# Kernel optimization log

Measured on AMD Instinct MI355X. Metric: run time of the kernel, lower is better.

The kernel has to match this reference:

```python
import jax, jax.numpy as jnp
import numpy as np

BN_EPS = 1e-5

def _conv1x1(x, w, b):
    # x: [B,C,H,W], w: [O,C], b: [O] -> [B,O,H,W]
    return jnp.einsum('bchw,oc->bohw', x, w) + b[None, :, None, None]

def setup_inputs() -> dict:
    key = jax.random.key(0)
    ks = jax.random.split(key, 9)
    B, C, H, W = 8, 256, 64, 64
    I = C // 2
    s_in = 1.0 / np.sqrt(C)
    s_out = 1.0 / np.sqrt(I)
    return {
        'x':       jax.random.normal(ks[0], (B, C, H, W), dtype=jnp.float32),
        'g_w':     jax.random.uniform(ks[1], (I, C), jnp.float32, -s_in, s_in),
        'g_b':     jax.random.uniform(ks[2], (I,),  jnp.float32, -s_in, s_in),
        'theta_w': jax.random.uniform(ks[3], (I, C), jnp.float32, -s_in, s_in),
        'theta_b': jax.random.uniform(ks[4], (I,),  jnp.float32, -s_in, s_in),
        'phi_w':   jax.random.uniform(ks[5], (I, C), jnp.float32, -s_in, s_in),
        'phi_b':   jax.random.uniform(ks[6], (I,),  jnp.float32, -s_in, s_in),
        'w_w':     jax.random.uniform(ks[7], (C, I), jnp.float32, -s_out, s_out),
        'w_b':     jax.random.uniform(ks[8], (C,),  jnp.float32, -s_out, s_out),
        'gamma':   jnp.ones((C,), dtype=jnp.float32),   # BN weight init constant 1
        'beta':    jnp.zeros((C,), dtype=jnp.float32),  # BN bias init constant 0
    }

def reference(x, g_w, g_b, theta_w, theta_b, phi_w, phi_b, w_w, w_b, gamma, beta):
    B, C, H, W = x.shape
    I = g_w.shape[0]
    N = H * W
    g_x     = _conv1x1(x, g_w, g_b).reshape(B, I, N)          # [B,I,N]
    theta_x = _conv1x1(x, theta_w, theta_b).reshape(B, I, N)  # [B,I,N]
    phi_x   = _conv1x1(x, phi_w, phi_b).reshape(B, I, N)      # [B,I,N]
    # f = theta^T @ phi : [B,N,N]
    f = jnp.einsum('bin,bim->bnm', theta_x, phi_x)
    a = jax.nn.softmax(f, axis=-1)
    # y = a @ g^T : [B,N,I] -> [B,I,H,W]
    y = jnp.einsum('bnm,bim->bin', a, g_x).reshape(B, I, H, W)
    wy = _conv1x1(y, w_w, w_b)                                # [B,C,H,W]
    # BatchNorm2d (training mode: batch statistics over B,H,W per channel)
    mean = jnp.mean(wy, axis=(0, 2, 3), keepdims=True)
    var = jnp.var(wy, axis=(0, 2, 3), keepdims=True)
    wy_bn = (wy - mean) * jax.lax.rsqrt(var + BN_EPS)
    wy_bn = wy_bn * gamma[None, :, None, None] + beta[None, :, None, None]
    return wy_bn + x
```

## Files before the change

kernel.cpp:

```cpp
#include <hip/hip_runtime.h>

#define B_ 8
#define C_ 256
#define I_ 128
#define N_ 4096
#define BN_ (B_ * N_)
#define LOG2E 1.4426950408889634f

typedef __attribute__((ext_vector_type(8))) short bf16x8;
typedef __attribute__((ext_vector_type(4))) float f32x4;
typedef __attribute__((ext_vector_type(4))) int i32x4;

static __device__ __forceinline__ short f2bf(float f) {
    unsigned u = __float_as_uint(f);
    unsigned r = u + 0x7fffu + ((u >> 16) & 1u);
    return (short)(r >> 16);
}
static __device__ __forceinline__ float bf2f(short s) {
    return __uint_as_float(((unsigned)(unsigned short)s) << 16);
}
static __device__ __forceinline__ unsigned cvt_pk_bf16(float lo, float hi) {
    unsigned r;
    asm("v_cvt_pk_bf16_f32 %0, %1, %2" : "=v"(r) : "v"(lo), "v"(hi));
    return r;
}

__global__ void k_prep(const float* g_w, const float* theta_w, const float* phi_w,
                       const float* g_b, const float* theta_b, const float* phi_b,
                       const float* w_w, short* wcat, short* wwb, float* bcat) {
    int i = blockIdx.x * 256 + threadIdx.x;
    if (i < 384 * 256) {
        int j = i >> 8, c = i & 255;
        float v = (j < 128) ? theta_w[j * 256 + c] * LOG2E
                : (j < 256) ? phi_w[(j - 128) * 256 + c]
                            : g_w[(j - 256) * 256 + c];
        wcat[i] = f2bf(v);
    } else if (i < 384 * 256 + 256 * 128) {
        int k = i - 384 * 256;
        wwb[k] = f2bf(w_w[k]);
    } else if (i < 384 * 256 + 256 * 128 + 384) {
        int j = i - (384 * 256 + 256 * 128);
        bcat[j] = (j < 128) ? theta_b[j] * LOG2E
                : (j < 256) ? phi_b[j - 128] : g_b[j - 256];
    }
}

__global__ __launch_bounds__(256) void k_proj(const float* __restrict__ x,
                                              const short* __restrict__ wcat,
                                              const float* __restrict__ bcat,
                                              short* __restrict__ tp,
                                              short* __restrict__ gmat) {
    int b = blockIdx.y;
    int n0 = blockIdx.x * 64;
    int tid = threadIdx.x;
    int wave = tid >> 6, lane = tid & 63, s = lane & 15, q = lane >> 4;
    __shared__ short xs[64][264];

#pragma unroll
    for (int it = 0; it < 16; ++it) {
        int cr = (tid >> 4) + it * 16;
        int nc = tid & 15;
        const float4 v = *(const float4*)&x[((size_t)b * C_ + cr) * N_ + n0 + nc * 4];
        xs[nc * 4 + 0][cr] = f2bf(v.x);
        xs[nc * 4 + 1][cr] = f2bf(v.y);
        xs[nc * 4 + 2][cr] = f2bf(v.z);
        xs[nc * 4 + 3][cr] = f2bf(v.w);
    }
    __syncthreads();

    f32x4 acc[4][6];
#pragma unroll
    for (int rt = 0; rt < 4; ++rt)
#pragma unroll
        for (int jt = 0; jt < 6; ++jt) acc[rt][jt] = (f32x4){0.f, 0.f, 0.f, 0.f};

#pragma unroll
    for (int kb = 0; kb < 8; ++kb) {
        bf16x8 af[4], bfv[6];
#pragma unroll
        for (int rt = 0; rt < 4; ++rt)
            af[rt] = *(const bf16x8*)&xs[rt * 16 + s][kb * 32 + q * 8];
#pragma unroll
        for (int jt = 0; jt < 6; ++jt)
            bfv[jt] = *(const bf16x8*)&wcat[(wave * 96 + jt * 16 + s) * 256 + kb * 32 + q * 8];
#pragma unroll
        for (int rt = 0; rt < 4; ++rt)
#pragma unroll
            for (int jt = 0; jt < 6; ++jt)
                acc[rt][jt] = __builtin_amdgcn_mfma_f32_16x16x32_bf16(af[rt], bfv[jt], acc[rt][jt], 0, 0, 0);
    }

#pragma unroll
    for (int rt = 0; rt < 4; ++rt)
#pragma unroll
        for (int jt = 0; jt < 6; ++jt) {
            int j = wave * 96 + jt * 16 + s;
            float bias = bcat[j];
#pragma unroll
            for (int r = 0; r < 4; ++r) {
                int n = n0 + rt * 16 + 4 * q + r;
                float v = acc[rt][jt][r] + bias;
                if (j < 256)
                    tp[((size_t)b * N_ + n) * 256 + j] = f2bf(v);
                else
                    gmat[((size_t)b * I_ + (j - 256)) * N_ + n] = f2bf(v);
            }
        }
}

__global__ __launch_bounds__(256, 2) void k_attn(const short* __restrict__ tp,
                                                 const short* __restrict__ gmat,
                                                 float* __restrict__ Op,
                                                 float* __restrict__ lbuf) {
    int id = blockIdx.x;
    int b = id & 7;
    int qt = (id >> 3) & 31;
    int half = id >> 8;
    int n0 = qt * 128;
    int tid = threadIdx.x;
    int wave = tid >> 6, lane = tid & 63, s = lane & 15, q = lane >> 4;

    __shared__ __align__(16) short Kt[128 * 128];
    __shared__ __align__(16) short Vt[128 * 128];

    char* KtB = (char*)Kt;
    char* VtB = (char*)Vt;

    const int swz = (s & 7) << 4;
    int kA[4];
#pragma unroll
    for (int kb = 0; kb < 4; ++kb) kA[kb] = s * 256 + ((kb * 64 + q * 16) ^ swz);
    int vA[2];
#pragma unroll
    for (int kb2 = 0; kb2 < 2; ++kb2)
        vA[kb2] = s * 256 + ((kb2 * 64 + q * 16) ^ swz);
    int krow = tid >> 4, kch = tid & 15;
    int stW = krow * 256 + ((kch * 16) ^ ((krow & 7) << 4));

    bf16x8 qf[2][4];
#pragma unroll
    for (int fr = 0; fr < 2; ++fr) {
        const short* qb = tp + ((size_t)b * N_ + n0 + wave * 32 + fr * 16 + s) * 256;
#pragma unroll
        for (int kb = 0; kb < 4; ++kb) qf[fr][kb] = *(const bf16x8*)(qb + kb * 32 + q * 8);
    }

    f32x4 ot[2][8];
#pragma unroll
    for (int fr = 0; fr < 2; ++fr)
#pragma unroll
        for (int t = 0; t < 8; ++t) ot[fr][t] = (f32x4){0.f, 0.f, 0.f, 0.f};
    float lsum[2] = {0.f, 0.f};

    const int mStart = half * 2048, mEnd = mStart + 2048;

    bf16x8 pk[8], pv[8];
#pragma unroll
    for (int it = 0; it < 8; ++it) {
        pk[it] = *(const bf16x8*)&tp[((size_t)b * N_ + mStart + krow + it * 16) * 256 + 128 + kch * 8];
        pv[it] = *(const bf16x8*)&gmat[((size_t)b * I_ + krow + it * 16) * N_ + mStart + kch * 8];
    }

    for (int m0 = mStart; m0 < mEnd; m0 += 128) {
        __syncthreads();
#pragma unroll
        for (int it = 0; it < 8; ++it) {
            *(bf16x8*)(KtB + stW + it * 4096) = pk[it];
            *(bf16x8*)(VtB + stW + it * 4096) = pv[it];
        }
        __syncthreads();
        if (m0 + 128 < mEnd) {
#pragma unroll
            for (int it = 0; it < 8; ++it) {
                pk[it] = *(const bf16x8*)&tp[((size_t)b * N_ + m0 + 128 + krow + it * 16) * 256 + 128 + kch * 8];
                pv[it] = *(const bf16x8*)&gmat[((size_t)b * I_ + krow + it * 16) * N_ + m0 + 128 + kch * 8];
            }
        }

#pragma unroll
        for (int h = 0; h < 2; ++h) {
            const int hK = h * 16384;
            const int hV = h * 128;

            f32x4 sa[2][4];
#pragma unroll
            for (int fr = 0; fr < 2; ++fr)
#pragma unroll
                for (int tc = 0; tc < 4; ++tc) sa[fr][tc] = (f32x4){0.f, 0.f, 0.f, 0.f};
            __builtin_amdgcn_s_setprio(1);
#pragma unroll
            for (int tc = 0; tc < 4; ++tc) {
                bf16x8 bfv[4];
#pragma unroll
                for (int kb = 0; kb < 4; ++kb)
                    bfv[kb] = *(const bf16x8*)(KtB + hK + kA[kb] + tc * 4096);
#pragma unroll
                for (int fr = 0; fr < 2; ++fr)
#pragma unroll
                    for (int kb = 0; kb < 4; ++kb)
                        sa[fr][tc] = __builtin_amdgcn_mfma_f32_16x16x32_bf16(bfv[kb], qf[fr][kb], sa[fr][tc], 0, 0, 0);
            }
            __builtin_amdgcn_s_setprio(0);

            unsigned W[2][4][2];
#pragma unroll
            for (int fr = 0; fr < 2; ++fr) {
#pragma unroll
                for (int tc = 0; tc < 4; ++tc)
#pragma unroll
                    for (int r = 0; r < 4; ++r) sa[fr][tc][r] = exp2f(sa[fr][tc][r]);
                float t0 = (sa[fr][0][0] + sa[fr][0][1]) + (sa[fr][0][2] + sa[fr][0][3]);
                float t1 = (sa[fr][1][0] + sa[fr][1][1]) + (sa[fr][1][2] + sa[fr][1][3]);
                float t2 = (sa[fr][2][0] + sa[fr][2][1]) + (sa[fr][2][2] + sa[fr][2][3]);
                float t3 = (sa[fr][3][0] + sa[fr][3][1]) + (sa[fr][3][2] + sa[fr][3][3]);
                lsum[fr] += (t0 + t1) + (t2 + t3);
#pragma unroll
                for (int tc = 0; tc < 4; ++tc) {
                    W[fr][tc][0] = cvt_pk_bf16(sa[fr][tc][0], sa[fr][tc][1]);
                    W[fr][tc][1] = cvt_pk_bf16(sa[fr][tc][2], sa[fr][tc][3]);
                }
            }

#pragma unroll
            for (int kb2 = 0; kb2 < 2; ++kb2) {
                bf16x8 pa[2];
#pragma unroll
                for (int fr = 0; fr < 2; ++fr) {
                    unsigned rA = W[fr][2 * kb2 + 0][0];
                    unsigned rB = W[fr][2 * kb2 + 0][1];
                    unsigned rC = W[fr][2 * kb2 + 1][0];
                    unsigned rD = W[fr][2 * kb2 + 1][1];
                    asm("v_permlane32_swap_b32 %0, %1" : "+v"(rA), "+v"(rC));
                    asm("v_permlane32_swap_b32 %0, %1" : "+v"(rB), "+v"(rD));
                    asm("v_permlane16_swap_b32 %0, %1" : "+v"(rA), "+v"(rC));
                    asm("v_permlane16_swap_b32 %0, %1" : "+v"(rB), "+v"(rD));
                    i32x4 wv = (i32x4){(int)rA, (int)rB, (int)rC, (int)rD};
                    pa[fr] = __builtin_bit_cast(bf16x8, wv);
                }
                __builtin_amdgcn_s_setprio(1);
#pragma unroll
                for (int t = 0; t < 8; ++t) {
                    bf16x8 vb = *(const bf16x8*)(VtB + hV + vA[kb2] + t * 4096);
                    ot[0][t] = __builtin_amdgcn_mfma_f32_16x16x32_bf16(pa[0], vb, ot[0][t], 0, 0, 0);
                    ot[1][t] = __builtin_amdgcn_mfma_f32_16x16x32_bf16(pa[1], vb, ot[1][t], 0, 0, 0);
                }
                __builtin_amdgcn_s_setprio(0);
            }
        }
    }

#pragma unroll
    for (int fr = 0; fr < 2; ++fr) {
        lsum[fr] += __shfl_xor(lsum[fr], 16);
        lsum[fr] += __shfl_xor(lsum[fr], 32);
    }
    if (q == 0) {
#pragma unroll
        for (int fr = 0; fr < 2; ++fr) {
            size_t row = (size_t)half * BN_ + (size_t)b * N_ + n0 + wave * 32 + fr * 16 + s;
            lbuf[row] = lsum[fr];
        }
    }

#pragma unroll
    for (int fr = 0; fr < 2; ++fr) {
        size_t rbase = (size_t)half * BN_ + (size_t)b * N_ + n0 + wave * 32 + fr * 16 + 4 * q;
#pragma unroll
        for (int t = 0; t < 8; ++t)
#pragma unroll
            for (int r = 0; r < 4; ++r)
                Op[(rbase + r) * I_ + t * 16 + s] = ot[fr][t][r];
    }
}

__global__ __launch_bounds__(256) void k_wy(const float* __restrict__ Op,
                                            const float* __restrict__ lbuf,
                                            const short* __restrict__ wwb,
                                            const float* __restrict__ w_b,
                                            short* __restrict__ wyh) {
    int b = blockIdx.y;
    int n0 = blockIdx.x * 64;
    int tid = threadIdx.x;
    int wave = tid >> 6, lane = tid & 63, s = lane & 15, q = lane >> 4;

    float linv[4];
#pragma unroll
    for (int nt = 0; nt < 4; ++nt) {
        size_t rn = (size_t)b * N_ + n0 + nt * 16 + s;
        linv[nt] = 1.0f / (lbuf[rn] + lbuf[(size_t)BN_ + rn]);
    }

    f32x4 acc[4][4];
#pragma unroll
    for (int ct = 0; ct < 4; ++ct)
#pragma unroll
        for (int nt = 0; nt < 4; ++nt) acc[ct][nt] = (f32x4){0.f, 0.f, 0.f, 0.f};
#pragma unroll
    for (int kb = 0; kb < 4; ++kb) {
        bf16x8 af[4], bfv[4];
#pragma unroll
        for (int ct = 0; ct < 4; ++ct)
            af[ct] = *(const bf16x8*)&wwb[(wave * 64 + ct * 16 + s) * 128 + kb * 32 + q * 8];
#pragma unroll
        for (int nt = 0; nt < 4; ++nt) {
            size_t rn = (size_t)b * N_ + n0 + nt * 16 + s;
            const float* p1 = Op + rn * I_ + kb * 32 + q * 8;
            const float* p2 = p1 + (size_t)BN_ * I_;
            float4 a0 = *(const float4*)p1;
            float4 a1 = *(const float4*)(p1 + 4);
            float4 b0 = *(const float4*)p2;
            float4 b1 = *(const float4*)(p2 + 4);
            short v[8];
            v[0] = f2bf((a0.x + b0.x) * linv[nt]);
            v[1] = f2bf((a0.y + b0.y) * linv[nt]);
            v[2] = f2bf((a0.z + b0.z) * linv[nt]);
            v[3] = f2bf((a0.w + b0.w) * linv[nt]);
            v[4] = f2bf((a1.x + b1.x) * linv[nt]);
            v[5] = f2bf((a1.y + b1.y) * linv[nt]);
            v[6] = f2bf((a1.z + b1.z) * linv[nt]);
            v[7] = f2bf((a1.w + b1.w) * linv[nt]);
            bfv[nt] = *(const bf16x8*)v;
        }
#pragma unroll
        for (int ct = 0; ct < 4; ++ct)
#pragma unroll
            for (int nt = 0; nt < 4; ++nt)
                acc[ct][nt] = __builtin_amdgcn_mfma_f32_16x16x32_bf16(af[ct], bfv[nt], acc[ct][nt], 0, 0, 0);
    }
#pragma unroll
    for (int ct = 0; ct < 4; ++ct)
#pragma unroll
        for (int nt = 0; nt < 4; ++nt)
#pragma unroll
            for (int r = 0; r < 4; ++r) {
                int c = wave * 64 + ct * 16 + 4 * q + r;
                int n = n0 + nt * 16 + s;
                wyh[((size_t)b * C_ + c) * N_ + n] = f2bf(acc[ct][nt][r] + w_b[c]);
            }
}

__global__ __launch_bounds__(256) void k_stats(const short* __restrict__ wyh,
                                               const float* __restrict__ gamma,
                                               const float* __restrict__ beta,
                                               float* __restrict__ scale,
                                               float* __restrict__ shift) {
    int c = blockIdx.x;
    int tid = threadIdx.x;
    float s1 = 0.f, s2 = 0.f;
    for (int b = 0; b < B_; ++b) {
        const short* p = wyh + ((size_t)b * C_ + c) * N_;
        for (int idx = tid * 8; idx < N_; idx += 2048) {
            bf16x8 v = *(const bf16x8*)&p[idx];
#pragma unroll
            for (int j = 0; j < 8; ++j) {
                float f = bf2f(v[j]);
                s1 += f;
                s2 += f * f;
            }
        }
    }
#pragma unroll
    for (int off = 1; off < 64; off <<= 1) {
        s1 += __shfl_xor(s1, off);
        s2 += __shfl_xor(s2, off);
    }
    __shared__ float r1[4], r2[4];
    if ((tid & 63) == 0) { r1[tid >> 6] = s1; r2[tid >> 6] = s2; }
    __syncthreads();
    if (tid == 0) {
        float t1 = r1[0] + r1[1] + r1[2] + r1[3];
        float t2 = r2[0] + r2[1] + r2[2] + r2[3];
        const float inv = 1.0f / 32768.0f;
        float mean = t1 * inv;
        float var = t2 * inv - mean * mean;
        float sc = gamma[c] * rsqrtf(var + 1e-5f);
        scale[c] = sc;
        shift[c] = beta[c] - mean * sc;
    }
}

__global__ __launch_bounds__(256) void k_out(const short* __restrict__ wyh,
                                             const float* __restrict__ x,
                                             const float* __restrict__ scale,
                                             const float* __restrict__ shift,
                                             float* __restrict__ out) {
    int gid = blockIdx.x * 256 + threadIdx.x;
    size_t base = (size_t)gid * 8;
    int c = (int)((base >> 12) & 255);
    float sc = scale[c], sh = shift[c];
    bf16x8 w = *(const bf16x8*)&wyh[base];
    float4 x0 = *(const float4*)&x[base];
    float4 x1 = *(const float4*)&x[base + 4];
    float4 o0, o1;
    o0.x = bf2f(w[0]) * sc + sh + x0.x;
    o0.y = bf2f(w[1]) * sc + sh + x0.y;
    o0.z = bf2f(w[2]) * sc + sh + x0.z;
    o0.w = bf2f(w[3]) * sc + sh + x0.w;
    o1.x = bf2f(w[4]) * sc + sh + x1.x;
    o1.y = bf2f(w[5]) * sc + sh + x1.y;
    o1.z = bf2f(w[6]) * sc + sh + x1.z;
    o1.w = bf2f(w[7]) * sc + sh + x1.w;
    *(float4*)&out[base] = o0;
    *(float4*)&out[base + 4] = o1;
}

extern "C" void kernel_launch(void* const* d_in, const int* in_sizes, int n_in,
                              void* d_out, int out_size, void* d_ws, size_t ws_size,
                              hipStream_t stream) {
    const float* x       = (const float*)d_in[0];
    const float* g_w     = (const float*)d_in[1];
    const float* g_b     = (const float*)d_in[2];
    const float* theta_w = (const float*)d_in[3];
    const float* theta_b = (const float*)d_in[4];
    const float* phi_w   = (const float*)d_in[5];
    const float* phi_b   = (const float*)d_in[6];
    const float* w_w     = (const float*)d_in[7];
    const float* w_b     = (const float*)d_in[8];
    const float* gamma   = (const float*)d_in[9];
    const float* beta    = (const float*)d_in[10];

    char* ws = (char*)d_ws;
    size_t off = 0;
    auto alloc = [&](size_t bytes) {
        void* p = ws + off;
        off += (bytes + 255) & ~(size_t)255;
        return p;
    };
    short*  wcat  = (short*)alloc((size_t)384 * 256 * 2);
    short*  wwb   = (short*)alloc((size_t)256 * 128 * 2);
    float*  bcat  = (float*)alloc((size_t)384 * 4);
    float*  scale = (float*)alloc(256 * 4);
    float*  shift = (float*)alloc(256 * 4);
    short*  tp    = (short*)alloc((size_t)BN_ * 256 * 2);
    short*  gmat  = (short*)alloc((size_t)B_ * I_ * N_ * 2);
    short*  wyh   = (short*)alloc((size_t)BN_ * C_ * 2);
    float*  lbuf  = (float*)alloc((size_t)2 * BN_ * 4);
    float*  Op    = (float*)d_out;

    k_prep<<<514, 256, 0, stream>>>(g_w, theta_w, phi_w, g_b, theta_b, phi_b, w_w,
                                    wcat, wwb, bcat);
    k_proj<<<dim3(64, 8), 256, 0, stream>>>(x, wcat, bcat, tp, gmat);
    k_attn<<<512, 256, 0, stream>>>(tp, gmat, Op, lbuf);
    k_wy<<<dim3(64, 8), 256, 0, stream>>>(Op, lbuf, wwb, w_b, wyh);
    k_stats<<<256, 256, 0, stream>>>(wyh, gamma, beta, scale, shift);
    k_out<<<4096, 256, 0, stream>>>(wyh, x, scale, shift, (float*)d_out);
}
```

Measured before the change: 265.8 us.

## Fuse attention with output projection and drop the split-KV fp32 partials

```diff
diff --git a/kernel.cpp b/kernel.cpp
--- a/kernel.cpp
+++ b/kernel.cpp
@@ -108,23 +108,21 @@
         }
 }
 
-__global__ __launch_bounds__(256, 2) void k_attn(const short* __restrict__ tp,
-                                                 const short* __restrict__ gmat,
-                                                 float* __restrict__ Op,
-                                                 float* __restrict__ lbuf) {
+__global__ __launch_bounds__(512, 2) void k_attn_wy(const short* __restrict__ tp,
+                                                    const short* __restrict__ gmat,
+                                                    const short* __restrict__ wwb,
+                                                    const float* __restrict__ w_b,
+                                                    short* __restrict__ wyh) {
     int id = blockIdx.x;
     int b = id & 7;
-    int qt = (id >> 3) & 31;
-    int half = id >> 8;
+    int qt = id >> 3;
     int n0 = qt * 128;
     int tid = threadIdx.x;
     int wave = tid >> 6, lane = tid & 63, s = lane & 15, q = lane >> 4;
 
-    __shared__ __align__(16) short Kt[128 * 128];
-    __shared__ __align__(16) short Vt[128 * 128];
-
-    char* KtB = (char*)Kt;
-    char* VtB = (char*)Vt;
+    __shared__ __align__(16) short SH[65536];
+    __shared__ float l_lds[128];
+    char* base = (char*)SH;
 
     const int swz = (s & 7) << 4;
     int kA[4];
@@ -132,211 +130,163 @@
     for (int kb = 0; kb < 4; ++kb) kA[kb] = s * 256 + ((kb * 64 + q * 16) ^ swz);
     int vA[2];
 #pragma unroll
-    for (int kb2 = 0; kb2 < 2; ++kb2)
-        vA[kb2] = s * 256 + ((kb2 * 64 + q * 16) ^ swz);
+    for (int kb2 = 0; kb2 < 2; ++kb2) vA[kb2] = s * 256 + ((kb2 * 64 + q * 16) ^ swz);
     int krow = tid >> 4, kch = tid & 15;
     int stW = krow * 256 + ((kch * 16) ^ ((krow & 7) << 4));
 
-    bf16x8 qf[2][4];
-#pragma unroll
-    for (int fr = 0; fr < 2; ++fr) {
-        const short* qb = tp + ((size_t)b * N_ + n0 + wave * 32 + fr * 16 + s) * 256;
-#pragma unroll
-        for (int kb = 0; kb < 4; ++kb) qf[fr][kb] = *(const bf16x8*)(qb + kb * 32 + q * 8);
-    }
-
-    f32x4 ot[2][8];
-#pragma unroll
-    for (int fr = 0; fr < 2; ++fr)
-#pragma unroll
-        for (int t = 0; t < 8; ++t) ot[fr][t] = (f32x4){0.f, 0.f, 0.f, 0.f};
-    float lsum[2] = {0.f, 0.f};
-
-    const int mStart = half * 2048, mEnd = mStart + 2048;
-
-    bf16x8 pk[8], pv[8];
-#pragma unroll
-    for (int it = 0; it < 8; ++it) {
-        pk[it] = *(const bf16x8*)&tp[((size_t)b * N_ + mStart + krow + it * 16) * 256 + 128 + kch * 8];
-        pv[it] = *(const bf16x8*)&gmat[((size_t)b * I_ + krow + it * 16) * N_ + mStart + kch * 8];
-    }
-
-    for (int m0 = mStart; m0 < mEnd; m0 += 128) {
-        __syncthreads();
-#pragma unroll
-        for (int it = 0; it < 8; ++it) {
-            *(bf16x8*)(KtB + stW + it * 4096) = pk[it];
-            *(bf16x8*)(VtB + stW + it * 4096) = pv[it];
-        }
-        __syncthreads();
-        if (m0 + 128 < mEnd) {
-#pragma unroll
-            for (int it = 0; it < 8; ++it) {
-                pk[it] = *(const bf16x8*)&tp[((size_t)b * N_ + m0 + 128 + krow + it * 16) * 256 + 128 + kch * 8];
-                pv[it] = *(const bf16x8*)&gmat[((size_t)b * I_ + krow + it * 16) * N_ + m0 + 128 + kch * 8];
+    bf16x8 qf[4];
+    {
+        const short* qb = tp + ((size_t)b * N_ + n0 + wave * 16 + s) * 256;
+#pragma unroll
+        for (int kb = 0; kb < 4; ++kb) qf[kb] = *(const bf16x8*)(qb + kb * 32 + q * 8);
+    }
+
+    f32x4 ot[8];
+#pragma unroll
+    for (int t = 0; t < 8; ++t) ot[t] = (f32x4){0.f, 0.f, 0.f, 0.f};
+    float lsum = 0.f;
+
+    bf16x8 pk[4], pv[4];
+#pragma unroll
+    for (int it = 0; it < 4; ++it) {
+        pk[it] = *(const bf16x8*)&tp[((size_t)b * N_ + krow + it * 32) * 256 + 128 + kch * 8];
+        pv[it] = *(const bf16x8*)&gmat[((size_t)b * I_ + krow + it * 32) * N_ + kch * 8];
+    }
+#pragma unroll
+    for (int it = 0; it < 4; ++it) {
+        *(bf16x8*)(base + stW + it * 8192) = pk[it];
+        *(bf16x8*)(base + 32768 + stW + it * 8192) = pv[it];
+    }
+    __syncthreads();
+
+    for (int i = 0; i < 32; ++i) {
+        char* KtB = base + (i & 1) * 65536;
+        char* VtB = KtB + 32768;
+        if (i < 31) {
+            int m = (i + 1) * 128;
+#pragma unroll
+            for (int it = 0; it < 4; ++it) {
+                pk[it] = *(const bf16x8*)&tp[((size_t)b * N_ + m + krow + it * 32) * 256 + 128 + kch * 8];
+                pv[it] = *(const bf16x8*)&gmat[((size_t)b * I_ + krow + it * 32) * N_ + m + kch * 8];
             }
         }
 
 #pragma unroll
         for (int h = 0; h < 2; ++h) {
-            const int hK = h * 16384;
-            const int hV = h * 128;
-
-            f32x4 sa[2][4];
-#pragma unroll
-            for (int fr = 0; fr < 2; ++fr)
-#pragma unroll
-                for (int tc = 0; tc < 4; ++tc) sa[fr][tc] = (f32x4){0.f, 0.f, 0.f, 0.f};
+            const int hK = h * 16384, hV = h * 128;
+
+            f32x4 sa[4];
+#pragma unroll
+            for (int tc = 0; tc < 4; ++tc) sa[tc] = (f32x4){0.f, 0.f, 0.f, 0.f};
             __builtin_amdgcn_s_setprio(1);
 #pragma unroll
             for (int tc = 0; tc < 4; ++tc) {
-                bf16x8 bfv[4];
-#pragma unroll
-                for (int kb = 0; kb < 4; ++kb)
-                    bfv[kb] = *(const bf16x8*)(KtB + hK + kA[kb] + tc * 4096);
-#pragma unroll
-                for (int fr = 0; fr < 2; ++fr)
-#pragma unroll
-                    for (int kb = 0; kb < 4; ++kb)
-                        sa[fr][tc] = __builtin_amdgcn_mfma_f32_16x16x32_bf16(bfv[kb], qf[fr][kb], sa[fr][tc], 0, 0, 0);
+#pragma unroll
+                for (int kb = 0; kb < 4; ++kb) {
+                    bf16x8 bfv = *(const bf16x8*)(KtB + hK + kA[kb] + tc * 4096);
+                    sa[tc] = __builtin_amdgcn_mfma_f32_16x16x32_bf16(bfv, qf[kb], sa[tc], 0, 0, 0);
+                }
             }
             __builtin_amdgcn_s_setprio(0);
 
-            unsigned W[2][4][2];
-#pragma unroll
-            for (int fr = 0; fr < 2; ++fr) {
-#pragma unroll
-                for (int tc = 0; tc < 4; ++tc)
-#pragma unroll
-                    for (int r = 0; r < 4; ++r) sa[fr][tc][r] = exp2f(sa[fr][tc][r]);
-                float t0 = (sa[fr][0][0] + sa[fr][0][1]) + (sa[fr][0][2] + sa[fr][0][3]);
-                float t1 = (sa[fr][1][0] + sa[fr][1][1]) + (sa[fr][1][2] + sa[fr][1][3]);
-                float t2 = (sa[fr][2][0] + sa[fr][2][1]) + (sa[fr][2][2] + sa[fr][2][3]);
-                float t3 = (sa[fr][3][0] + sa[fr][3][1]) + (sa[fr][3][2] + sa[fr][3][3]);
-                lsum[fr] += (t0 + t1) + (t2 + t3);
-#pragma unroll
-                for (int tc = 0; tc < 4; ++tc) {
-                    W[fr][tc][0] = cvt_pk_bf16(sa[fr][tc][0], sa[fr][tc][1]);
-                    W[fr][tc][1] = cvt_pk_bf16(sa[fr][tc][2], sa[fr][tc][3]);
-                }
+#pragma unroll
+            for (int tc = 0; tc < 4; ++tc)
+#pragma unroll
+                for (int r = 0; r < 4; ++r) sa[tc][r] = exp2f(sa[tc][r]);
+            {
+                float t0 = (sa[0][0] + sa[0][1]) + (sa[0][2] + sa[0][3]);
+                float t1 = (sa[1][0] + sa[1][1]) + (sa[1][2] + sa[1][3]);
+                float t2 = (sa[2][0] + sa[2][1]) + (sa[2][2] + sa[2][3]);
+                float t3 = (sa[3][0] + sa[3][1]) + (sa[3][2] + sa[3][3]);
+                lsum += (t0 + t1) + (t2 + t3);
+            }
+            unsigned W[4][2];
+#pragma unroll
+            for (int tc = 0; tc < 4; ++tc) {
+                W[tc][0] = cvt_pk_bf16(sa[tc][0], sa[tc][1]);
+                W[tc][1] = cvt_pk_bf16(sa[tc][2], sa[tc][3]);
             }
 
 #pragma unroll
             for (int kb2 = 0; kb2 < 2; ++kb2) {
-                bf16x8 pa[2];
-#pragma unroll
-                for (int fr = 0; fr < 2; ++fr) {
-                    unsigned rA = W[fr][2 * kb2 + 0][0];
-                    unsigned rB = W[fr][2 * kb2 + 0][1];
-                    unsigned rC = W[fr][2 * kb2 + 1][0];
-                    unsigned rD = W[fr][2 * kb2 + 1][1];
-                    asm("v_permlane32_swap_b32 %0, %1" : "+v"(rA), "+v"(rC));
-                    asm("v_permlane32_swap_b32 %0, %1" : "+v"(rB), "+v"(rD));
-                    asm("v_permlane16_swap_b32 %0, %1" : "+v"(rA), "+v"(rC));
-                    asm("v_permlane16_swap_b32 %0, %1" : "+v"(rB), "+v"(rD));
-                    i32x4 wv = (i32x4){(int)rA, (int)rB, (int)rC, (int)rD};
-                    pa[fr] = __builtin_bit_cast(bf16x8, wv);
-                }
+                unsigned rA = W[2 * kb2 + 0][0];
+                unsigned rB = W[2 * kb2 + 0][1];
+                unsigned rC = W[2 * kb2 + 1][0];
+                unsigned rD = W[2 * kb2 + 1][1];
+                asm("v_permlane32_swap_b32 %0, %1" : "+v"(rA), "+v"(rC));
+                asm("v_permlane32_swap_b32 %0, %1" : "+v"(rB), "+v"(rD));
+                asm("v_permlane16_swap_b32 %0, %1" : "+v"(rA), "+v"(rC));
+                asm("v_permlane16_swap_b32 %0, %1" : "+v"(rB), "+v"(rD));
+                i32x4 wv = (i32x4){(int)rA, (int)rB, (int)rC, (int)rD};
+                bf16x8 pa = __builtin_bit_cast(bf16x8, wv);
                 __builtin_amdgcn_s_setprio(1);
 #pragma unroll
                 for (int t = 0; t < 8; ++t) {
                     bf16x8 vb = *(const bf16x8*)(VtB + hV + vA[kb2] + t * 4096);
-                    ot[0][t] = __builtin_amdgcn_mfma_f32_16x16x32_bf16(pa[0], vb, ot[0][t], 0, 0, 0);
-                    ot[1][t] = __builtin_amdgcn_mfma_f32_16x16x32_bf16(pa[1], vb, ot[1][t], 0, 0, 0);
+                    ot[t] = __builtin_amdgcn_mfma_f32_16x16x32_bf16(pa, vb, ot[t], 0, 0, 0);
                 }
                 __builtin_amdgcn_s_setprio(0);
             }
         }
-    }
-
-#pragma unroll
-    for (int fr = 0; fr < 2; ++fr) {
-        lsum[fr] += __shfl_xor(lsum[fr], 16);
-        lsum[fr] += __shfl_xor(lsum[fr], 32);
-    }
-    if (q == 0) {
-#pragma unroll
-        for (int fr = 0; fr < 2; ++fr) {
-            size_t row = (size_t)half * BN_ + (size_t)b * N_ + n0 + wave * 32 + fr * 16 + s;
-            lbuf[row] = lsum[fr];
-        }
-    }
-
-#pragma unroll
-    for (int fr = 0; fr < 2; ++fr) {
-        size_t rbase = (size_t)half * BN_ + (size_t)b * N_ + n0 + wave * 32 + fr * 16 + 4 * q;
-#pragma unroll
-        for (int t = 0; t < 8; ++t)
-#pragma unroll
-            for (int r = 0; r < 4; ++r)
-                Op[(rbase + r) * I_ + t * 16 + s] = ot[fr][t][r];
-    }
-}
-
-__global__ __launch_bounds__(256) void k_wy(const float* __restrict__ Op,
-                                            const float* __restrict__ lbuf,
-                                            const short* __restrict__ wwb,
-                                            const float* __restrict__ w_b,
-                                            short* __restrict__ wyh) {
-    int b = blockIdx.y;
-    int n0 = blockIdx.x * 64;
-    int tid = threadIdx.x;
-    int wave = tid >> 6, lane = tid & 63, s = lane & 15, q = lane >> 4;
-
-    float linv[4];
-#pragma unroll
-    for (int nt = 0; nt < 4; ++nt) {
-        size_t rn = (size_t)b * N_ + n0 + nt * 16 + s;
-        linv[nt] = 1.0f / (lbuf[rn] + lbuf[(size_t)BN_ + rn]);
-    }
-
-    f32x4 acc[4][4];
-#pragma unroll
-    for (int ct = 0; ct < 4; ++ct)
-#pragma unroll
-        for (int nt = 0; nt < 4; ++nt) acc[ct][nt] = (f32x4){0.f, 0.f, 0.f, 0.f};
+
+        if (i < 31) {
+            char* KtN = base + ((i & 1) ^ 1) * 65536;
+#pragma unroll
+            for (int it = 0; it < 4; ++it) {
+                *(bf16x8*)(KtN + stW + it * 8192) = pk[it];
+                *(bf16x8*)(KtN + 32768 + stW + it * 8192) = pv[it];
+            }
+        }
+        __syncthreads();
+    }
+
+    lsum += __shfl_xor(lsum, 16);
+    lsum += __shfl_xor(lsum, 32);
+    if (lane < 16) l_lds[wave * 16 + s] = lsum;
+
+#pragma unroll
+    for (int t = 0; t < 8; ++t)
+#pragma unroll
+        for (int r = 0; r < 4; ++r) {
+            int row = wave * 16 + 4 * q + r;
+            int byt = row * 256 + (((t * 16 + s) * 2) ^ ((row & 7) << 4));
+            *(short*)(base + byt) = f2bf(ot[t][r]);
+        }
+    __syncthreads();
+
+    f32x4 acc[2][8];
+#pragma unroll
+    for (int ct = 0; ct < 2; ++ct)
+#pragma unroll
+        for (int jt = 0; jt < 8; ++jt) acc[ct][jt] = (f32x4){0.f, 0.f, 0.f, 0.f};
 #pragma unroll
     for (int kb = 0; kb < 4; ++kb) {
-        bf16x8 af[4], bfv[4];
-#pragma unroll
-        for (int ct = 0; ct < 4; ++ct)
-            af[ct] = *(const bf16x8*)&wwb[(wave * 64 + ct * 16 + s) * 128 + kb * 32 + q * 8];
-#pragma unroll
-        for (int nt = 0; nt < 4; ++nt) {
-            size_t rn = (size_t)b * N_ + n0 + nt * 16 + s;
-            const float* p1 = Op + rn * I_ + kb * 32 + q * 8;
-            const float* p2 = p1 + (size_t)BN_ * I_;
-            float4 a0 = *(const float4*)p1;
-            float4 a1 = *(const float4*)(p1 + 4);
-            float4 b0 = *(const float4*)p2;
-            float4 b1 = *(const float4*)(p2 + 4);
-            short v[8];
-            v[0] = f2bf((a0.x + b0.x) * linv[nt]);
-            v[1] = f2bf((a0.y + b0.y) * linv[nt]);
-            v[2] = f2bf((a0.z + b0.z) * linv[nt]);
-            v[3] = f2bf((a0.w + b0.w) * linv[nt]);
-            v[4] = f2bf((a1.x + b1.x) * linv[nt]);
-            v[5] = f2bf((a1.y + b1.y) * linv[nt]);
-            v[6] = f2bf((a1.z + b1.z) * linv[nt]);
-            v[7] = f2bf((a1.w + b1.w) * linv[nt]);
-            bfv[nt] = *(const bf16x8*)v;
-        }
-#pragma unroll
-        for (int ct = 0; ct < 4; ++ct)
-#pragma unroll
-            for (int nt = 0; nt < 4; ++nt)
-                acc[ct][nt] = __builtin_amdgcn_mfma_f32_16x16x32_bf16(af[ct], bfv[nt], acc[ct][nt], 0, 0, 0);
-    }
-#pragma unroll
-    for (int ct = 0; ct < 4; ++ct)
-#pragma unroll
-        for (int nt = 0; nt < 4; ++nt)
-#pragma unroll
-            for (int r = 0; r < 4; ++r) {
-                int c = wave * 64 + ct * 16 + 4 * q + r;
-                int n = n0 + nt * 16 + s;
-                wyh[((size_t)b * C_ + c) * N_ + n] = f2bf(acc[ct][nt][r] + w_b[c]);
-            }
+        bf16x8 af[2];
+#pragma unroll
+        for (int ct = 0; ct < 2; ++ct)
+            af[ct] = *(const bf16x8*)&wwb[(wave * 32 + ct * 16 + s) * 128 + kb * 32 + q * 8];
+#pragma unroll
+        for (int jt = 0; jt < 8; ++jt) {
+            bf16x8 yb = *(const bf16x8*)(base + kA[kb] + jt * 4096);
+#pragma unroll
+            for (int ct = 0; ct < 2; ++ct)
+                acc[ct][jt] = __builtin_amdgcn_mfma_f32_16x16x32_bf16(af[ct], yb, acc[ct][jt], 0, 0, 0);
+        }
+    }
+    float linv[8];
+#pragma unroll
+    for (int jt = 0; jt < 8; ++jt) linv[jt] = 1.0f / l_lds[jt * 16 + s];
+#pragma unroll
+    for (int ct = 0; ct < 2; ++ct)
+#pragma unroll
+        for (int r = 0; r < 4; ++r) {
+            int c = wave * 32 + ct * 16 + 4 * q + r;
+            float bias = w_b[c];
+#pragma unroll
+            for (int jt = 0; jt < 8; ++jt)
+                wyh[((size_t)b * C_ + c) * N_ + n0 + jt * 16 + s] =
+                    f2bf(acc[ct][jt][r] * linv[jt] + bias);
+        }
 }
 
 __global__ __launch_bounds__(256) void k_stats(const short* __restrict__ wyh,
@@ -434,14 +384,11 @@
     short*  tp    = (short*)alloc((size_t)BN_ * 256 * 2);
     short*  gmat  = (short*)alloc((size_t)B_ * I_ * N_ * 2);
     short*  wyh   = (short*)alloc((size_t)BN_ * C_ * 2);
-    float*  lbuf  = (float*)alloc((size_t)2 * BN_ * 4);
-    float*  Op    = (float*)d_out;
 
     k_prep<<<514, 256, 0, stream>>>(g_w, theta_w, phi_w, g_b, theta_b, phi_b, w_w,
                                     wcat, wwb, bcat);
     k_proj<<<dim3(64, 8), 256, 0, stream>>>(x, wcat, bcat, tp, gmat);
-    k_attn<<<512, 256, 0, stream>>>(tp, gmat, Op, lbuf);
-    k_wy<<<dim3(64, 8), 256, 0, stream>>>(Op, lbuf, wwb, w_b, wyh);
+    k_attn_wy<<<256, 512, 0, stream>>>(tp, gmat, wwb, w_b, wyh);
     k_stats<<<256, 256, 0, stream>>>(wyh, gamma, beta, scale, shift);
     k_out<<<4096, 256, 0, stream>>>(wyh, x, scale, shift, (float*)d_out);
 }
```

Measured after the change: 236.4 us. -11.0%, faster.
